# Performance work log

Hardware: AMD Instinct MI355X
Metric: run time of the kernel (lower is better)

Reference implementation:

```python
import jax, jax.numpy as jnp
import numpy as np

B, T, D = 32, 1024, 1024
N, L = 77, 768
H = 8
TED = 2048  # time_embed_dim
EPS = 1e-5


def _ln(x, g, b):
    m = jnp.mean(x, axis=-1, keepdims=True)
    v = jnp.var(x, axis=-1, keepdims=True)
    return (x - m) * jax.lax.rsqrt(v + EPS) * g + b


def setup_inputs() -> dict:
    key = jax.random.key(0)
    ks = jax.random.split(key, 16)
    s = lambda fan_in: 1.0 / np.sqrt(fan_in)
    return {
        "x": jax.random.normal(ks[0], (B, T, D), jnp.float32),
        "xf": jax.random.normal(ks[1], (B, N, L), jnp.float32),
        "emb": jax.random.normal(ks[2], (B, TED), jnp.float32),
        "norm_g": jnp.ones((D,), jnp.float32),
        "norm_b": jnp.zeros((D,), jnp.float32),
        "tnorm_g": jnp.ones((L,), jnp.float32),
        "tnorm_b": jnp.zeros((L,), jnp.float32),
        "Wq": jax.random.normal(ks[3], (D, D), jnp.float32) * s(D),
        "bq": jnp.zeros((D,), jnp.float32),
        "Wk": jax.random.normal(ks[4], (L, D), jnp.float32) * s(L),
        "bk": jnp.zeros((D,), jnp.float32),
        "Wv": jax.random.normal(ks[5], (L, D), jnp.float32) * s(L),
        "bv": jnp.zeros((D,), jnp.float32),
        "emb_W": jax.random.normal(ks[6], (TED, 2 * D), jnp.float32) * s(TED),
        "emb_b": jnp.zeros((2 * D,), jnp.float32),
        "onorm_g": jnp.ones((D,), jnp.float32),
        "onorm_b": jnp.zeros((D,), jnp.float32),
        "Wo": jax.random.normal(ks[7], (D, D), jnp.float32) * s(D),
        "bo": jnp.zeros((D,), jnp.float32),
    }


def reference(x, xf, emb, norm_g, norm_b, tnorm_g, tnorm_b, Wq, bq, Wk, bk, Wv, bv,
              emb_W, emb_b, onorm_g, onorm_b, Wo, bo):
    Bc, Tc, Dc = x.shape
    Nc = xf.shape[1]
    hd = Dc // H
    # projections
    q = _ln(x, norm_g, norm_b) @ Wq + bq                      # [B,T,D]
    xfn = _ln(xf, tnorm_g, tnorm_b)                           # [B,N,L]
    k = (xfn @ Wk + bk).reshape(Bc, Nc, H, hd)                # [B,N,H,hd]
    v = (xfn @ Wv + bv).reshape(Bc, Nc, H, hd)                # [B,N,H,hd]
    q = jax.nn.softmax(q.reshape(Bc, Tc, H, hd), axis=-1)     # softmax over head_dim
    k = jax.nn.softmax(k, axis=1)                             # softmax over N (key tokens)
    # linear-attention: no TxN matrix
    attn = jnp.einsum('bnhd,bnhl->bhdl', k, v)                # [B,H,hd,hd]
    y = jnp.einsum('bthd,bhdl->bthl', q, attn).reshape(Bc, Tc, Dc)
    # StylizationBlock
    emb_out = jax.nn.silu(emb) @ emb_W + emb_b                # [B,2D]
    scale, shift = jnp.split(emb_out[:, None, :], 2, axis=2)  # [B,1,D] each
    h = _ln(y, onorm_g, onorm_b) * (1.0 + scale) + shift
    h = jax.nn.silu(h) @ Wo + bo
    return x + h
```

## Files before the change

kernel.cpp:

```cpp
#include <hip/hip_runtime.h>
#include <hip/hip_bf16.h>
#include <math.h>

namespace {

constexpr int Bc  = 32;
constexpr int Tc  = 1024;
constexpr int Dc  = 1024;
constexpr int Nt  = 77;
constexpr int Lc  = 768;
constexpr int HDc = 128;
constexpr int TEDc = 2048;
constexpr float EPSc = 1e-5f;

typedef __attribute__((ext_vector_type(8))) short bf16x8;
typedef __attribute__((ext_vector_type(8))) unsigned short u16x8;
typedef __attribute__((ext_vector_type(4))) float f32x4;

__device__ __forceinline__ float silu_f(float x) { return x / (1.f + __expf(-x)); }

__device__ __forceinline__ unsigned short f2bf(float f) {
  unsigned u = __float_as_uint(f);
  return (unsigned short)((u + 0x7fffu + ((u >> 16) & 1u)) >> 16);
}
__device__ __forceinline__ float bf2f(unsigned short h) {
  return __uint_as_float(((unsigned)h) << 16);
}

__device__ __forceinline__ void gload16(const void* g, void* l) {
  __builtin_amdgcn_global_load_lds((const __attribute__((address_space(1))) void*)g,
                                   (__attribute__((address_space(3))) void*)l, 16, 0, 0);
}

__global__ __launch_bounds__(256) void ln_bf16_kernel(
    const float* __restrict__ src, unsigned short* __restrict__ dst, int cols,
    const float* __restrict__ g, const float* __restrict__ b)
{
  const int row = blockIdx.x;
  const float* p = src + (size_t)row * cols;
  const int c = threadIdx.x * 4;
  float4 v = make_float4(0.f, 0.f, 0.f, 0.f);
  if (c < cols) v = *reinterpret_cast<const float4*>(p + c);
  float s  = v.x + v.y + v.z + v.w;
  float sq = v.x * v.x + v.y * v.y + v.z * v.z + v.w * v.w;
  __shared__ float red[2][4];
  __shared__ float mr[2];
  for (int o = 32; o > 0; o >>= 1) { s += __shfl_down(s, o); sq += __shfl_down(sq, o); }
  const int wid = threadIdx.x >> 6, lane = threadIdx.x & 63;
  if (lane == 0) { red[0][wid] = s; red[1][wid] = sq; }
  __syncthreads();
  if (threadIdx.x == 0) {
    const float S  = red[0][0] + red[0][1] + red[0][2] + red[0][3];
    const float SQ = red[1][0] + red[1][1] + red[1][2] + red[1][3];
    const float mean = S / cols;
    const float var  = SQ / cols - mean * mean;
    mr[0] = mean; mr[1] = rsqrtf(var + EPSc);
  }
  __syncthreads();
  if (c < cols) {
    const float mean = mr[0], rstd = mr[1];
    ushort4 o;
    o.x = f2bf((v.x - mean) * rstd * g[c + 0] + b[c + 0]);
    o.y = f2bf((v.y - mean) * rstd * g[c + 1] + b[c + 1]);
    o.z = f2bf((v.z - mean) * rstd * g[c + 2] + b[c + 2]);
    o.w = f2bf((v.w - mean) * rstd * g[c + 3] + b[c + 3]);
    *reinterpret_cast<ushort4*>(dst + (size_t)row * cols + c) = o;
  }
}

__global__ __launch_bounds__(256) void convT_bf16_kernel(
    const float* __restrict__ W, unsigned short* __restrict__ Wt, int K, int N)
{
  __shared__ float t[32][33];
  const int n0 = blockIdx.x * 32, k0 = blockIdx.y * 32;
  const int tx = threadIdx.x & 31, ty = threadIdx.x >> 5;
  #pragma unroll
  for (int dy = 0; dy < 32; dy += 8)
    t[ty + dy][tx] = W[(size_t)(k0 + ty + dy) * N + n0 + tx];
  __syncthreads();
  #pragma unroll
  for (int dy = 0; dy < 32; dy += 8)
    Wt[(size_t)(n0 + ty + dy) * K + k0 + tx] = f2bf(t[tx][ty + dy]);
}

template<int EPI>
__global__ __launch_bounds__(512) void gemm2_kernel(
    const unsigned short* __restrict__ A, const unsigned short* __restrict__ Bt,
    const float* __restrict__ bias, void* __restrict__ Cout,
    int M, int K, int N, const float* __restrict__ xres)
{
  constexpr int LDSE = (EPI == 2) ? 32768 : 24576;
  __shared__ unsigned short lds[LDSE];
  const int tid = threadIdx.x, wid = tid >> 6, lane = tid & 63;
  const int ntx = N >> 7;
  int swz = blockIdx.x;
  const int nwg = gridDim.x;
  if ((nwg & 7) == 0) { const int cpx = nwg >> 3; swz = (swz & 7) * cpx + (swz >> 3); }
  const int bx = swz % ntx, by = swz / ntx;
  const int bm0 = by << 8, bn0 = bx << 7;
  const int wr = wid >> 1, wc = wid & 1, lhi = lane >> 4, llo = lane & 15;

  const int srow = lane >> 2, scol = (lane & 3) * 8;
  int ar0 = bm0 + wid * 32 + srow;      if (ar0 >= M) ar0 = M - 1;
  int ar1 = bm0 + wid * 32 + 16 + srow; if (ar1 >= M) ar1 = M - 1;
  const int br = bn0 + wid * 16 + srow;
  const unsigned short* Ag0 = A  + (size_t)ar0 * K + scol;
  const unsigned short* Ag1 = A  + (size_t)ar1 * K + scol;
  const unsigned short* Bg  = Bt + (size_t)br  * K + scol;
  const int alc0 = (wid * 2) * 512, alc1 = (wid * 2 + 1) * 512, blc = wid * 512;
  const int aoff = wr * 2048 + llo * 32 + lhi * 8;
  const int boff = wc * 2048 + llo * 32 + lhi * 8;

  f32x4 acc[4][4] = {};
  const int nt = K >> 5;

  gload16(Ag0, &lds[alc0]);
  gload16(Ag1, &lds[alc1]);
  gload16(Bg,  &lds[16384 + blc]);
  __syncthreads();

  int cur = 0;
  for (int t = 1; t < nt; ++t) {
    const int nb = cur ^ 1;
    const int k0 = t << 5;
    gload16(Ag0 + k0, &lds[nb * 8192 + alc0]);
    gload16(Ag1 + k0, &lds[nb * 8192 + alc1]);
    gload16(Bg  + k0, &lds[16384 + nb * 4096 + blc]);
    bf16x8 a_[4], b_[4];
    #pragma unroll
    for (int mi = 0; mi < 4; mi++) a_[mi] = *(const bf16x8*)(&lds[cur * 8192 + aoff + mi * 512]);
    #pragma unroll
    for (int ni = 0; ni < 4; ni++) b_[ni] = *(const bf16x8*)(&lds[16384 + cur * 4096 + boff + ni * 512]);
    #pragma unroll
    for (int mi = 0; mi < 4; mi++)
      #pragma unroll
      for (int ni = 0; ni < 4; ni++)
        acc[mi][ni] = __builtin_amdgcn_mfma_f32_16x16x32_bf16(a_[mi], b_[ni], acc[mi][ni], 0, 0, 0);
    __syncthreads();
    cur = nb;
  }
  {
    bf16x8 a_[4], b_[4];
    #pragma unroll
    for (int mi = 0; mi < 4; mi++) a_[mi] = *(const bf16x8*)(&lds[cur * 8192 + aoff + mi * 512]);
    #pragma unroll
    for (int ni = 0; ni < 4; ni++) b_[ni] = *(const bf16x8*)(&lds[16384 + cur * 4096 + boff + ni * 512]);
    #pragma unroll
    for (int mi = 0; mi < 4; mi++)
      #pragma unroll
      for (int ni = 0; ni < 4; ni++)
        acc[mi][ni] = __builtin_amdgcn_mfma_f32_16x16x32_bf16(a_[mi], b_[ni], acc[mi][ni], 0, 0, 0);
  }

  if constexpr (EPI != 2) {
    #pragma unroll
    for (int mi = 0; mi < 4; mi++) {
      #pragma unroll
      for (int ni = 0; ni < 4; ni++) {
        const int col = bn0 + wc * 64 + ni * 16 + llo;
        const float bs = bias[col];
        #pragma unroll
        for (int r = 0; r < 4; r++) {
          const int row = bm0 + wr * 64 + mi * 16 + lhi * 4 + r;
          if (row < M) {
            float v = acc[mi][ni][r] + bs;
            if (EPI == 1) v += xres[(size_t)row * N + col];
            ((float*)Cout)[(size_t)row * N + col] = v;
          }
        }
      }
    }
  } else {
    __syncthreads();
    #pragma unroll
    for (int mi = 0; mi < 4; mi++) {
      #pragma unroll
      for (int ni = 0; ni < 4; ni++) {
        const int col = wc * 64 + ni * 16 + llo;
        const float bs = bias[bn0 + col];
        #pragma unroll
        for (int r = 0; r < 4; r++) {
          const int row = wr * 64 + mi * 16 + lhi * 4 + r;
          lds[row * 128 + (col ^ ((row & 7) << 3))] = f2bf(acc[mi][ni][r] + bs);
        }
      }
    }
    __syncthreads();
    const int row = tid >> 1, cb = (tid & 1) * 64;
    const int sw = (row & 7) << 3;
    float mx = -1e30f;
    #pragma unroll
    for (int g = 0; g < 8; g++) {
      u16x8 u = *(const u16x8*)(&lds[row * 128 + ((cb + g * 8) ^ sw)]);
      #pragma unroll
      for (int j = 0; j < 8; j++) mx = fmaxf(mx, bf2f(u[j]));
    }
    mx = fmaxf(mx, __shfl_xor(mx, 1));
    float ssum = 0.f;
    #pragma unroll
    for (int g = 0; g < 8; g++) {
      unsigned short* p = &lds[row * 128 + ((cb + g * 8) ^ sw)];
      u16x8 u = *(const u16x8*)p;
      u16x8 e;
      #pragma unroll
      for (int j = 0; j < 8; j++) {
        float ev = __expf(bf2f(u[j]) - mx);
        ssum += ev;
        e[j] = f2bf(ev);
      }
      *(u16x8*)p = e;
    }
    ssum += __shfl_xor(ssum, 1);
    const float inv = 1.f / ssum;
    unsigned short* Cb = (unsigned short*)Cout;
    #pragma unroll
    for (int g = 0; g < 8; g++) {
      u16x8 u = *(const u16x8*)(&lds[row * 128 + ((cb + g * 8) ^ sw)]);
      u16x8 o;
      #pragma unroll
      for (int j = 0; j < 8; j++) o[j] = f2bf(bf2f(u[j]) * inv);
      *(u16x8*)(&Cb[(size_t)(bm0 + row) * N + bn0 + cb + g * 8]) = o;
    }
  }
}

__global__ void softmax_k_kernel(float* __restrict__ k) {
  const int idx = blockIdx.x * blockDim.x + threadIdx.x;
  const int b = idx >> 10, d = idx & 1023;
  float* p = k + (size_t)b * Nt * Dc + d;
  float m = -1e30f;
  for (int n = 0; n < Nt; n++) m = fmaxf(m, p[(size_t)n * Dc]);
  float s = 0.f;
  for (int n = 0; n < Nt; n++) s += __expf(p[(size_t)n * Dc] - m);
  const float inv = 1.f / s;
  for (int n = 0; n < Nt; n++) p[(size_t)n * Dc] = __expf(p[(size_t)n * Dc] - m) * inv;
}

__global__ __launch_bounds__(256) void attn_einsum_kernel(
    const float* __restrict__ k, const float* __restrict__ v,
    unsigned short* __restrict__ attnT) {
  const int bh = blockIdx.x;
  const int b = bh >> 3, h = bh & 7;
  __shared__ float ks[Nt][HDc];
  __shared__ float vs[Nt][HDc];
  const float* kb = k + (size_t)b * Nt * Dc + h * HDc;
  const float* vb = v + (size_t)b * Nt * Dc + h * HDc;
  for (int i = threadIdx.x; i < Nt * HDc; i += 256) {
    const int n = i >> 7, d = i & 127;
    ks[n][d] = kb[(size_t)n * Dc + d];
    vs[n][d] = vb[(size_t)n * Dc + d];
  }
  __syncthreads();
  const int tx = threadIdx.x & 15, ty = threadIdx.x >> 4;
  float acc[8][8] = {};
  for (int n = 0; n < Nt; n++) {
    float a[8], w[8];
    #pragma unroll
    for (int i = 0; i < 8; i++) a[i] = vs[n][ty + 16 * i];
    #pragma unroll
    for (int j = 0; j < 8; j++) w[j] = ks[n][tx + 16 * j];
    #pragma unroll
    for (int i = 0; i < 8; i++)
      #pragma unroll
      for (int j = 0; j < 8; j++)
        acc[i][j] += a[i] * w[j];
  }
  unsigned short* ab = attnT + (size_t)bh * HDc * HDc;
  #pragma unroll
  for (int i = 0; i < 8; i++)
    #pragma unroll
    for (int j = 0; j < 8; j++)
      ab[(size_t)(ty + 16 * i) * HDc + tx + 16 * j] = f2bf(acc[i][j]);
}

__global__ __launch_bounds__(256) void y_mfma_kernel(
    unsigned short* __restrict__ q, const unsigned short* __restrict__ attnT)
{
  __shared__ unsigned short lds[16384];
  const int tid = threadIdx.x, wid = tid >> 6, lane = tid & 63;
  const int bh = blockIdx.y, b = bh >> 3, h = bh & 7;
  const int bm0 = blockIdx.x << 7;
  const int wr = wid >> 1, wc = wid & 1, lhi = lane >> 4, llo = lane & 15;

  unsigned short* Abase = q + ((size_t)b * Tc) * Dc + h * HDc;
  const unsigned short* Btb = attnT + (size_t)bh * HDc * HDc;

  const int srow = lane >> 2, scol = (lane & 3) * 8;
  const int ar0 = bm0 + wid * 32 + srow, ar1 = ar0 + 16;
  const int br0 = wid * 32 + srow,       br1 = br0 + 16;
  const unsigned short* Ag0 = Abase + (size_t)ar0 * Dc + scol;
  const unsigned short* Ag1 = Abase + (size_t)ar1 * Dc + scol;
  const unsigned short* Bg0 = Btb + (size_t)br0 * HDc + scol;
  const unsigned short* Bg1 = Btb + (size_t)br1 * HDc + scol;
  const int lc0 = (wid * 2 + 0) * 512, lc1 = (wid * 2 + 1) * 512;
  const int aoff = wr * 2048 + llo * 32 + lhi * 8;
  const int boff = wc * 2048 + llo * 32 + lhi * 8;

  f32x4 acc[4][4] = {};

  gload16(Ag0, &lds[lc0]);
  gload16(Ag1, &lds[lc1]);
  gload16(Bg0, &lds[8192 + lc0]);
  gload16(Bg1, &lds[8192 + lc1]);
  __syncthreads();

  int cur = 0;
  for (int t = 1; t < 4; ++t) {
    const int nb = cur ^ 1;
    const int k0 = t << 5;
    gload16(Ag0 + k0, &lds[nb * 4096 + lc0]);
    gload16(Ag1 + k0, &lds[nb * 4096 + lc1]);
    gload16(Bg0 + k0, &lds[8192 + nb * 4096 + lc0]);
    gload16(Bg1 + k0, &lds[8192 + nb * 4096 + lc1]);
    bf16x8 a_[4], b_[4];
    #pragma unroll
    for (int mi = 0; mi < 4; mi++) a_[mi] = *(const bf16x8*)(&lds[cur * 4096 + aoff + mi * 512]);
    #pragma unroll
    for (int ni = 0; ni < 4; ni++) b_[ni] = *(const bf16x8*)(&lds[8192 + cur * 4096 + boff + ni * 512]);
    #pragma unroll
    for (int mi = 0; mi < 4; mi++)
      #pragma unroll
      for (int ni = 0; ni < 4; ni++)
        acc[mi][ni] = __builtin_amdgcn_mfma_f32_16x16x32_bf16(a_[mi], b_[ni], acc[mi][ni], 0, 0, 0);
    __syncthreads();
    cur = nb;
  }
  {
    bf16x8 a_[4], b_[4];
    #pragma unroll
    for (int mi = 0; mi < 4; mi++) a_[mi] = *(const bf16x8*)(&lds[cur * 4096 + aoff + mi * 512]);
    #pragma unroll
    for (int ni = 0; ni < 4; ni++) b_[ni] = *(const bf16x8*)(&lds[8192 + cur * 4096 + boff + ni * 512]);
    #pragma unroll
    for (int mi = 0; mi < 4; mi++)
      #pragma unroll
      for (int ni = 0; ni < 4; ni++)
        acc[mi][ni] = __builtin_amdgcn_mfma_f32_16x16x32_bf16(a_[mi], b_[ni], acc[mi][ni], 0, 0, 0);
  }

  __syncthreads();
  #pragma unroll
  for (int mi = 0; mi < 4; mi++) {
    #pragma unroll
    for (int ni = 0; ni < 4; ni++) {
      const int col = wc * 64 + ni * 16 + llo;
      #pragma unroll
      for (int r = 0; r < 4; r++) {
        const int row = wr * 64 + mi * 16 + lhi * 4 + r;
        lds[row * 128 + (col ^ ((row & 7) << 3))] = f2bf(acc[mi][ni][r]);
      }
    }
  }
  __syncthreads();
  const int row = tid >> 1, cb = (tid & 1) * 64;
  const int sw = (row & 7) << 3;
  #pragma unroll
  for (int g = 0; g < 8; g++) {
    u16x8 u = *(const u16x8*)(&lds[row * 128 + ((cb + g * 8) ^ sw)]);
    *(u16x8*)(&Abase[(size_t)(bm0 + row) * Dc + cb + g * 8]) = u;
  }
}

__global__ __launch_bounds__(256) void ln_mod_silu_bf16_kernel(
    unsigned short* __restrict__ y, const float* __restrict__ ss,
    const float* __restrict__ g, const float* __restrict__ bvec) {
  const int row = blockIdx.x;
  const int b = row >> 10;
  unsigned short* p = y + (size_t)row * Dc;
  const int c = threadIdx.x * 4;
  ushort4 u = *reinterpret_cast<const ushort4*>(p + c);
  float vv[4] = {bf2f(u.x), bf2f(u.y), bf2f(u.z), bf2f(u.w)};
  float s  = vv[0] + vv[1] + vv[2] + vv[3];
  float sq = vv[0]*vv[0] + vv[1]*vv[1] + vv[2]*vv[2] + vv[3]*vv[3];
  __shared__ float red[2][4];
  __shared__ float mr[2];
  for (int o = 32; o > 0; o >>= 1) { s += __shfl_down(s, o); sq += __shfl_down(sq, o); }
  const int wid = threadIdx.x >> 6, lane = threadIdx.x & 63;
  if (lane == 0) { red[0][wid] = s; red[1][wid] = sq; }
  __syncthreads();
  if (threadIdx.x == 0) {
    const float S  = red[0][0] + red[0][1] + red[0][2] + red[0][3];
    const float SQ = red[1][0] + red[1][1] + red[1][2] + red[1][3];
    const float mean = S / Dc;
    const float var = SQ / Dc - mean * mean;
    mr[0] = mean; mr[1] = rsqrtf(var + EPSc);
  }
  __syncthreads();
  const float mean = mr[0], rstd = mr[1];
  const float* ssb = ss + (size_t)b * 2 * Dc;
  ushort4 o;
  float t0 = (vv[0] - mean) * rstd * g[c + 0] + bvec[c + 0];
  float t1 = (vv[1] - mean) * rstd * g[c + 1] + bvec[c + 1];
  float t2 = (vv[2] - mean) * rstd * g[c + 2] + bvec[c + 2];
  float t3 = (vv[3] - mean) * rstd * g[c + 3] + bvec[c + 3];
  o.x = f2bf(silu_f(t0 * (1.f + ssb[c + 0]) + ssb[Dc + c + 0]));
  o.y = f2bf(silu_f(t1 * (1.f + ssb[c + 1]) + ssb[Dc + c + 1]));
  o.z = f2bf(silu_f(t2 * (1.f + ssb[c + 2]) + ssb[Dc + c + 2]));
  o.w = f2bf(silu_f(t3 * (1.f + ssb[c + 3]) + ssb[Dc + c + 3]));
  *reinterpret_cast<ushort4*>(p + c) = o;
}

__global__ __launch_bounds__(256) void silu_emb_kernel(
    const float* __restrict__ emb, float* __restrict__ sile) {
  const int i = (blockIdx.x * 256 + threadIdx.x) * 4;
  float4 v = *reinterpret_cast<const float4*>(emb + i);
  v.x = silu_f(v.x); v.y = silu_f(v.y); v.z = silu_f(v.z); v.w = silu_f(v.w);
  *reinterpret_cast<float4*>(sile + i) = v;
}

__global__ __launch_bounds__(256) void emb_part_kernel(
    const float* __restrict__ sile, const float* __restrict__ W,
    float* __restrict__ part) {
  const int split = blockIdx.y;
  const int n = blockIdx.x * 256 + threadIdx.x;
  const int k0 = split * 64;
  const float* se = sile + k0;
  const float* Wp = W + (size_t)k0 * (2 * Dc) + n;
  float acc[32] = {};
  for (int kk = 0; kk < 64; kk++) {
    const float w = Wp[(size_t)kk * (2 * Dc)];
    #pragma unroll
    for (int m = 0; m < 32; m++)
      acc[m] = fmaf(se[m * TEDc + kk], w, acc[m]);
  }
  float* pp = part + (size_t)split * 32 * (2 * Dc) + n;
  #pragma unroll
  for (int m = 0; m < 32; m++) pp[(size_t)m * (2 * Dc)] = acc[m];
}

__global__ __launch_bounds__(256) void emb_reduce_kernel(
    const float* __restrict__ part, const float* __restrict__ bias,
    float* __restrict__ ssb) {
  const int i = blockIdx.x * 256 + threadIdx.x;
  const int n = i & (2 * Dc - 1);
  float s = bias[n];
  #pragma unroll 8
  for (int sp = 0; sp < 32; sp++) s += part[(size_t)sp * 32 * (2 * Dc) + i];
  ssb[i] = s;
}

}

extern "C" void kernel_launch(void* const* d_in, const int* in_sizes, int n_in,
                              void* d_out, int out_size, void* d_ws, size_t ws_size,
                              hipStream_t stream) {
  const float* x       = (const float*)d_in[0];
  const float* xf      = (const float*)d_in[1];
  const float* emb     = (const float*)d_in[2];
  const float* norm_g  = (const float*)d_in[3];
  const float* norm_b  = (const float*)d_in[4];
  const float* tnorm_g = (const float*)d_in[5];
  const float* tnorm_b = (const float*)d_in[6];
  const float* Wq      = (const float*)d_in[7];
  const float* bq      = (const float*)d_in[8];
  const float* Wk      = (const float*)d_in[9];
  const float* bk      = (const float*)d_in[10];
  const float* Wv      = (const float*)d_in[11];
  const float* bv_     = (const float*)d_in[12];
  const float* emb_W   = (const float*)d_in[13];
  const float* emb_b   = (const float*)d_in[14];
  const float* onorm_g = (const float*)d_in[15];
  const float* onorm_b = (const float*)d_in[16];
  const float* Wo      = (const float*)d_in[17];
  const float* bo      = (const float*)d_in[18];
  float* out = (float*)d_out;

  char* ws = (char*)d_ws;
  unsigned short* Ab = (unsigned short*)ws;
  char* R = ws;
  unsigned short* qb   = (unsigned short*)(ws + 67108864);
  unsigned short* Wq_t = (unsigned short*)(ws + 134217728);
  unsigned short* Wk_t = (unsigned short*)(ws + 136314880);
  unsigned short* Wv_t = (unsigned short*)(ws + 137887744);
  unsigned short* Wo_t = (unsigned short*)(ws + 139460608);
  float*          ssb  = (float*)(ws + 141557760);
  float*          sile = (float*)(ws + 141819904);
  float*          part = (float*)(ws + 142082048);
  unsigned short* xfb   = (unsigned short*)(R);
  float*          kbuf  = (float*)(R + 3784704);
  float*          vbuf  = (float*)(R + 13877248);
  unsigned short* attnT = (unsigned short*)(R + 23969792);

  const int Mq  = Bc * Tc;
  const int Mkv = Bc * Nt;

  ln_bf16_kernel<<<Mq, 256, 0, stream>>>(x, Ab, Dc, norm_g, norm_b);
  convT_bf16_kernel<<<dim3(Dc / 32, Dc / 32), 256, 0, stream>>>(Wq, Wq_t, Dc, Dc);
  convT_bf16_kernel<<<dim3(Dc / 32, Lc / 32), 256, 0, stream>>>(Wk, Wk_t, Lc, Dc);
  convT_bf16_kernel<<<dim3(Dc / 32, Lc / 32), 256, 0, stream>>>(Wv, Wv_t, Lc, Dc);
  convT_bf16_kernel<<<dim3(Dc / 32, Dc / 32), 256, 0, stream>>>(Wo, Wo_t, Dc, Dc);

  gemm2_kernel<2><<<(Dc / 128) * (Mq / 256), 512, 0, stream>>>(
      Ab, Wq_t, bq, qb, Mq, Dc, Dc, nullptr);

  ln_bf16_kernel<<<Mkv, 256, 0, stream>>>(xf, xfb, Lc, tnorm_g, tnorm_b);
  gemm2_kernel<0><<<(Dc / 128) * ((Mkv + 255) / 256), 512, 0, stream>>>(
      xfb, Wk_t, bk, kbuf, Mkv, Lc, Dc, nullptr);
  gemm2_kernel<0><<<(Dc / 128) * ((Mkv + 255) / 256), 512, 0, stream>>>(
      xfb, Wv_t, bv_, vbuf, Mkv, Lc, Dc, nullptr);
  softmax_k_kernel<<<(Bc * Dc) / 256, 256, 0, stream>>>(kbuf);
  attn_einsum_kernel<<<Bc * 8, 256, 0, stream>>>(kbuf, vbuf, attnT);

  silu_emb_kernel<<<(Bc * TEDc) / 1024, 256, 0, stream>>>(emb, sile);
  emb_part_kernel<<<dim3(8, 32), 256, 0, stream>>>(sile, emb_W, part);
  emb_reduce_kernel<<<(Bc * 2 * Dc) / 256, 256, 0, stream>>>(part, emb_b, ssb);

  y_mfma_kernel<<<dim3(Tc / 128, Bc * 8), 256, 0, stream>>>(qb, attnT);
  ln_mod_silu_bf16_kernel<<<Mq, 256, 0, stream>>>(qb, ssb, onorm_g, onorm_b);
  gemm2_kernel<1><<<(Dc / 128) * (Mq / 256), 512, 0, stream>>>(
      qb, Wo_t, bo, out, Mq, Dc, Dc, x);
}
```

Before: 499.5 us.

## Swizzle LDS tiles in MFMA GEMMs and fuse K/V projections into one GEMM

```diff
diff --git a/kernel.cpp b/kernel.cpp
--- a/kernel.cpp
+++ b/kernel.cpp
@@ -30,6 +30,10 @@
 __device__ __forceinline__ void gload16(const void* g, void* l) {
   __builtin_amdgcn_global_load_lds((const __attribute__((address_space(1))) void*)g,
                                    (__attribute__((address_space(3))) void*)l, 16, 0, 0);
+}
+
+__device__ __forceinline__ int rowswz(int r) {
+  return (((r >> 3) & 1) << 1) | ((r >> 1) & 1);
 }
 
 __global__ __launch_bounds__(256) void ln_bf16_kernel(
@@ -83,11 +87,29 @@
     Wt[(size_t)(n0 + ty + dy) * K + k0 + tx] = f2bf(t[tx][ty + dy]);
 }
 
+__global__ __launch_bounds__(256) void convT2_bf16_kernel(
+    const float* __restrict__ W0, unsigned short* __restrict__ T0,
+    const float* __restrict__ W1, unsigned short* __restrict__ T1, int K, int N)
+{
+  __shared__ float t[32][33];
+  const float* W = blockIdx.z ? W1 : W0;
+  unsigned short* Wt = blockIdx.z ? T1 : T0;
+  const int n0 = blockIdx.x * 32, k0 = blockIdx.y * 32;
+  const int tx = threadIdx.x & 31, ty = threadIdx.x >> 5;
+  #pragma unroll
+  for (int dy = 0; dy < 32; dy += 8)
+    t[ty + dy][tx] = W[(size_t)(k0 + ty + dy) * N + n0 + tx];
+  __syncthreads();
+  #pragma unroll
+  for (int dy = 0; dy < 32; dy += 8)
+    Wt[(size_t)(n0 + ty + dy) * K + k0 + tx] = f2bf(t[tx][ty + dy]);
+}
+
 template<int EPI>
 __global__ __launch_bounds__(512) void gemm2_kernel(
     const unsigned short* __restrict__ A, const unsigned short* __restrict__ Bt,
-    const float* __restrict__ bias, void* __restrict__ Cout,
-    int M, int K, int N, const float* __restrict__ xres)
+    const float* __restrict__ bias, const float* __restrict__ bias2, int bsplit,
+    void* __restrict__ Cout, int M, int K, int N, const float* __restrict__ xres)
 {
   constexpr int LDSE = (EPI == 2) ? 32768 : 24576;
   __shared__ unsigned short lds[LDSE];
@@ -100,7 +122,8 @@
   const int bm0 = by << 8, bn0 = bx << 7;
   const int wr = wid >> 1, wc = wid & 1, lhi = lane >> 4, llo = lane & 15;
 
-  const int srow = lane >> 2, scol = (lane & 3) * 8;
+  const int srow = lane >> 2;
+  const int scol = (((lane & 3) ^ rowswz(srow)) * 8);
   int ar0 = bm0 + wid * 32 + srow;      if (ar0 >= M) ar0 = M - 1;
   int ar1 = bm0 + wid * 32 + 16 + srow; if (ar1 >= M) ar1 = M - 1;
   const int br = bn0 + wid * 16 + srow;
@@ -108,8 +131,9 @@
   const unsigned short* Ag1 = A  + (size_t)ar1 * K + scol;
   const unsigned short* Bg  = Bt + (size_t)br  * K + scol;
   const int alc0 = (wid * 2) * 512, alc1 = (wid * 2 + 1) * 512, blc = wid * 512;
-  const int aoff = wr * 2048 + llo * 32 + lhi * 8;
-  const int boff = wc * 2048 + llo * 32 + lhi * 8;
+  const int rx = rowswz(llo);
+  const int aoff = wr * 2048 + llo * 32 + ((lhi ^ rx) * 8);
+  const int boff = wc * 2048 + llo * 32 + ((lhi ^ rx) * 8);
 
   f32x4 acc[4][4] = {};
   const int nt = K >> 5;
@@ -158,7 +182,7 @@
       #pragma unroll
       for (int ni = 0; ni < 4; ni++) {
         const int col = bn0 + wc * 64 + ni * 16 + llo;
-        const float bs = bias[col];
+        const float bs = (bsplit > 0 && col >= bsplit) ? bias2[col - bsplit] : bias[col];
         #pragma unroll
         for (int r = 0; r < 4; r++) {
           const int row = bm0 + wr * 64 + mi * 16 + lhi * 4 + r;
@@ -224,31 +248,30 @@
   }
 }
 
-__global__ void softmax_k_kernel(float* __restrict__ k) {
+__global__ void softmax_k_kernel(float* __restrict__ kv) {
   const int idx = blockIdx.x * blockDim.x + threadIdx.x;
   const int b = idx >> 10, d = idx & 1023;
-  float* p = k + (size_t)b * Nt * Dc + d;
+  float* p = kv + (size_t)b * Nt * 2048 + d;
   float m = -1e30f;
-  for (int n = 0; n < Nt; n++) m = fmaxf(m, p[(size_t)n * Dc]);
+  for (int n = 0; n < Nt; n++) m = fmaxf(m, p[(size_t)n * 2048]);
   float s = 0.f;
-  for (int n = 0; n < Nt; n++) s += __expf(p[(size_t)n * Dc] - m);
+  for (int n = 0; n < Nt; n++) s += __expf(p[(size_t)n * 2048] - m);
   const float inv = 1.f / s;
-  for (int n = 0; n < Nt; n++) p[(size_t)n * Dc] = __expf(p[(size_t)n * Dc] - m) * inv;
+  for (int n = 0; n < Nt; n++) p[(size_t)n * 2048] = __expf(p[(size_t)n * 2048] - m) * inv;
 }
 
 __global__ __launch_bounds__(256) void attn_einsum_kernel(
-    const float* __restrict__ k, const float* __restrict__ v,
-    unsigned short* __restrict__ attnT) {
+    const float* __restrict__ kv, unsigned short* __restrict__ attnT) {
   const int bh = blockIdx.x;
   const int b = bh >> 3, h = bh & 7;
   __shared__ float ks[Nt][HDc];
   __shared__ float vs[Nt][HDc];
-  const float* kb = k + (size_t)b * Nt * Dc + h * HDc;
-  const float* vb = v + (size_t)b * Nt * Dc + h * HDc;
+  const float* kb = kv + (size_t)b * Nt * 2048 + h * HDc;
+  const float* vb = kv + (size_t)b * Nt * 2048 + 1024 + h * HDc;
   for (int i = threadIdx.x; i < Nt * HDc; i += 256) {
     const int n = i >> 7, d = i & 127;
-    ks[n][d] = kb[(size_t)n * Dc + d];
-    vs[n][d] = vb[(size_t)n * Dc + d];
+    ks[n][d] = kb[(size_t)n * 2048 + d];
+    vs[n][d] = vb[(size_t)n * 2048 + d];
   }
   __syncthreads();
   const int tx = threadIdx.x & 15, ty = threadIdx.x >> 4;
@@ -285,7 +308,8 @@
   unsigned short* Abase = q + ((size_t)b * Tc) * Dc + h * HDc;
   const unsigned short* Btb = attnT + (size_t)bh * HDc * HDc;
 
-  const int srow = lane >> 2, scol = (lane & 3) * 8;
+  const int srow = lane >> 2;
+  const int scol = (((lane & 3) ^ rowswz(srow)) * 8);
   const int ar0 = bm0 + wid * 32 + srow, ar1 = ar0 + 16;
   const int br0 = wid * 32 + srow,       br1 = br0 + 16;
   const unsigned short* Ag0 = Abase + (size_t)ar0 * Dc + scol;
@@ -293,8 +317,9 @@
   const unsigned short* Bg0 = Btb + (size_t)br0 * HDc + scol;
   const unsigned short* Bg1 = Btb + (size_t)br1 * HDc + scol;
   const int lc0 = (wid * 2 + 0) * 512, lc1 = (wid * 2 + 1) * 512;
-  const int aoff = wr * 2048 + llo * 32 + lhi * 8;
-  const int boff = wc * 2048 + llo * 32 + lhi * 8;
+  const int rx = rowswz(llo);
+  const int aoff = wr * 2048 + llo * 32 + ((lhi ^ rx) * 8);
+  const int boff = wc * 2048 + llo * 32 + ((lhi ^ rx) * 8);
 
   f32x4 acc[4][4] = {};
 
@@ -477,8 +502,7 @@
   float*          sile = (float*)(ws + 141819904);
   float*          part = (float*)(ws + 142082048);
   unsigned short* xfb   = (unsigned short*)(R);
-  float*          kbuf  = (float*)(R + 3784704);
-  float*          vbuf  = (float*)(R + 13877248);
+  float*          kv    = (float*)(R + 3784704);
   unsigned short* attnT = (unsigned short*)(R + 23969792);
 
   const int Mq  = Bc * Tc;
@@ -486,20 +510,17 @@
 
   ln_bf16_kernel<<<Mq, 256, 0, stream>>>(x, Ab, Dc, norm_g, norm_b);
   convT_bf16_kernel<<<dim3(Dc / 32, Dc / 32), 256, 0, stream>>>(Wq, Wq_t, Dc, Dc);
-  convT_bf16_kernel<<<dim3(Dc / 32, Lc / 32), 256, 0, stream>>>(Wk, Wk_t, Lc, Dc);
-  convT_bf16_kernel<<<dim3(Dc / 32, Lc / 32), 256, 0, stream>>>(Wv, Wv_t, Lc, Dc);
+  convT2_bf16_kernel<<<dim3(Dc / 32, Lc / 32, 2), 256, 0, stream>>>(Wk, Wk_t, Wv, Wv_t, Lc, Dc);
   convT_bf16_kernel<<<dim3(Dc / 32, Dc / 32), 256, 0, stream>>>(Wo, Wo_t, Dc, Dc);
 
   gemm2_kernel<2><<<(Dc / 128) * (Mq / 256), 512, 0, stream>>>(
-      Ab, Wq_t, bq, qb, Mq, Dc, Dc, nullptr);
+      Ab, Wq_t, bq, nullptr, 0, qb, Mq, Dc, Dc, nullptr);
 
   ln_bf16_kernel<<<Mkv, 256, 0, stream>>>(xf, xfb, Lc, tnorm_g, tnorm_b);
-  gemm2_kernel<0><<<(Dc / 128) * ((Mkv + 255) / 256), 512, 0, stream>>>(
-      xfb, Wk_t, bk, kbuf, Mkv, Lc, Dc, nullptr);
-  gemm2_kernel<0><<<(Dc / 128) * ((Mkv + 255) / 256), 512, 0, stream>>>(
-      xfb, Wv_t, bv_, vbuf, Mkv, Lc, Dc, nullptr);
-  softmax_k_kernel<<<(Bc * Dc) / 256, 256, 0, stream>>>(kbuf);
-  attn_einsum_kernel<<<Bc * 8, 256, 0, stream>>>(kbuf, vbuf, attnT);
+  gemm2_kernel<0><<<(2048 / 128) * ((Mkv + 255) / 256), 512, 0, stream>>>(
+      xfb, Wk_t, bk, bv_, 1024, kv, Mkv, Lc, 2048, nullptr);
+  softmax_k_kernel<<<(Bc * Dc) / 256, 256, 0, stream>>>(kv);
+  attn_einsum_kernel<<<Bc * 8, 256, 0, stream>>>(kv, attnT);
 
   silu_emb_kernel<<<(Bc * TEDc) / 1024, 256, 0, stream>>>(emb, sile);
   emb_part_kernel<<<dim3(8, 32), 256, 0, stream>>>(sile, emb_W, part);
@@ -508,5 +529,5 @@
   y_mfma_kernel<<<dim3(Tc / 128, Bc * 8), 256, 0, stream>>>(qb, attnT);
   ln_mod_silu_bf16_kernel<<<Mq, 256, 0, stream>>>(qb, ssb, onorm_g, onorm_b);
   gemm2_kernel<1><<<(Dc / 128) * (Mq / 256), 512, 0, stream>>>(
-      qb, Wo_t, bo, out, Mq, Dc, Dc, x);
-}
+      qb, Wo_t, bo, nullptr, 0, out, Mq, Dc, Dc, x);
+}
```

After: 481.6 us. -3.6%, faster.
